# Optimization experiments

Measured on AMD Instinct MI355X. Metric: run time of the kernel, lower is better.

The kernel has to match this reference:

```python
import jax, jax.numpy as jnp
import numpy as np

B, C, H, W = 4, 128, 128, 128
E, K, HID = 11, 6, 512  # num_experts, active_experts, 4*dim


def setup_inputs() -> dict:
    key = jax.random.key(0)
    ks = jax.random.split(key, 5)
    return {
        "x": jax.random.normal(ks[0], (B, C, H, W), jnp.float32),
        "gate_w": jax.random.normal(ks[1], (E, C), jnp.float32) * 0.02,
        "gate_b": jnp.zeros((E,), jnp.float32),
        "w1": jax.random.normal(ks[2], (E, HID, C), jnp.float32) * 0.02,
        "b1": jnp.zeros((E, HID), jnp.float32),
        "w2": jax.random.normal(ks[3], (E, C, HID), jnp.float32) * 0.02,
        "b2": jnp.zeros((E, C), jnp.float32),
    }


def reference(x, gate_w, gate_b, w1, b1, w2, b2):
    n_experts = gate_w.shape[0]
    k = K  # active_experts
    # channels-last for per-pixel routing / 1x1-conv-as-matmul
    xcl = jnp.transpose(x, (0, 2, 3, 1))  # [B,H,W,C]
    # --- router (1x1 conv gate + softmax over experts + top-k) ---
    logits = jnp.einsum('bhwc,ec->bhwe', xcl, gate_w) + gate_b
    scores = jax.nn.softmax(logits, axis=-1)            # [B,H,W,E]
    topk_p, topk_i = jax.lax.top_k(scores, k)           # [B,H,W,K]
    topk_p = topk_p / topk_p.sum(axis=-1, keepdims=True)
    # scatter routing weights into dense per-expert mask (indices distinct)
    onehot = jax.nn.one_hot(topk_i, n_experts, dtype=x.dtype)  # [B,H,W,K,E]
    mask = jnp.einsum('bhwke,bhwk->bhwe', onehot, topk_p)      # [B,H,W,E]
    # --- dense expert compute, masked accumulate (as in original loop) ---
    acc = jnp.zeros_like(xcl)
    for e in range(n_experts):
        h = jax.nn.gelu(jnp.einsum('bhwc,dc->bhwd', xcl, w1[e]) + b1[e],
                        approximate=False)  # torch GELU is exact erf form
        oe = jnp.einsum('bhwd,cd->bhwc', h, w2[e]) + b2[e]
        acc = acc + mask[..., e:e + 1] * oe
    y = x + jnp.transpose(acc, (0, 3, 1, 2))  # back to NCHW
    # --- load-balancing aux loss ---
    mean_prob = scores.mean(axis=(0, 1, 2))            # [E]
    mean_load = onehot.sum(axis=3).mean(axis=(0, 1, 2))  # binary mask mean, [E]
    aux_loss = n_experts * jnp.sum(mean_prob * mean_load)
    return (y, aux_loss)
```

## Files before the change

### kernel.cpp

```cpp
#include <hip/hip_runtime.h>
#include <stdint.h>

#define C_   128
#define HW_  16384
#define CHW_ (C_*HW_)
#define N_   65536
#define E_   11
#define K_   6
#define HID_ 512

typedef __attribute__((ext_vector_type(8))) _Float16 half8;
typedef __attribute__((ext_vector_type(2))) _Float16 h2;
typedef __attribute__((ext_vector_type(2))) __fp16 fp16v2;
typedef __attribute__((ext_vector_type(16))) float float16v;
typedef __attribute__((ext_vector_type(2))) unsigned uint2v;

#define GLD(g, s) __builtin_amdgcn_global_load_lds( \
    (const __attribute__((address_space(1))) unsigned int*)(uintptr_t)(g), \
    (__attribute__((address_space(3))) unsigned int*)(unsigned int)(uintptr_t)(s), 16, 0, 0)

__device__ __forceinline__ h2 pkrtz(float a, float b){
  union { fp16v2 f; h2 h; } u;
  u.f = __builtin_amdgcn_cvt_pkrtz(a, b);
  return u.h;
}
__device__ __forceinline__ h2 gelu2h(h2 v, h2 wr2){
  h2 u = v * v;
  h2 s = u * (h2)(_Float16)(-0.00076957f) + (h2)(_Float16)(0.0147811f);
  s = s * u + (h2)(_Float16)(-0.126434f);
  s = s * u + (h2)(_Float16)(0.795742f);
  h2 p = v * s;
  h2 phi = p * (h2)(_Float16)(0.5f) + (h2)(_Float16)(0.5f);
  return v * wr2 * phi;
}
__device__ __forceinline__ void pswap32(unsigned &a, unsigned &b){
#if __has_builtin(__builtin_amdgcn_permlane32_swap)
  uint2v r = __builtin_amdgcn_permlane32_swap(a, b, false, false);
  a = r.x; b = r.y;
#else
  asm volatile("v_permlane32_swap_b32 %0, %1" : "+v"(a), "+v"(b));
#endif
}

__global__ __launch_bounds__(256) void k_convert(const float* __restrict__ w1,
                                                 const float* __restrict__ w2,
                                                 const float* __restrict__ b1,
                                                 unsigned short* __restrict__ wimg,
                                                 unsigned short* __restrict__ b1h,
                                                 float* __restrict__ auxsum){
  int t = blockIdx.x * 256 + threadIdx.x;
  if (t < 23) auxsum[t] = 0.0f;
  if (t >= 185856) return;
  if (t >= 180224){
    int t2 = t - 180224;
    int rec = t2 >> 5, j5 = t2 & 31;
    int hi = j5 >> 4, j = j5 & 15;
    int e = rec >> 4, hc = rec & 15;
    int row = (j & 3) + 8 * (j >> 2) + 4 * hi;
    union { _Float16 h; unsigned short u; } cv;
    cv.h = (_Float16)b1[e * 512 + hc * 32 + row];
    b1h[rec * 32 + j5] = cv.u;
    return;
  }
  const float* src;
  size_t dst;
  if (t < 90112){
    int e = t >> 13, hid = (t >> 4) & 511, c8 = t & 15;
    src = w1 + (size_t)t * 8;
    int rec = e * 16 + (hid >> 5);
    int kc = c8 >> 1, half = c8 & 1;
    int l = (hid & 31) | (half << 5);
    dst = (size_t)rec * 8192 + kc * 512 + l * 8;
  } else {
    int u = t - 90112;
    int e = u >> 13, cc = (u >> 6) & 127, hd8 = u & 63;
    src = w2 + (size_t)u * 8;
    int rec = e * 16 + (hd8 >> 2);
    int kc2 = (hd8 >> 1) & 1, half = hd8 & 1, ct = cc >> 5;
    int l = (cc & 31) | (half << 5);
    dst = (size_t)rec * 8192 + 4096 + (ct * 2 + kc2) * 512 + l * 8;
  }
  float4 a = *(const float4*)src, b = *(const float4*)(src + 4);
  union { _Float16 h[8]; uint4 v; } u4;
  u4.h[0] = (_Float16)a.x; u4.h[1] = (_Float16)a.y;
  u4.h[2] = (_Float16)a.z; u4.h[3] = (_Float16)a.w;
  u4.h[4] = (_Float16)b.x; u4.h[5] = (_Float16)b.y;
  u4.h[6] = (_Float16)b.z; u4.h[7] = (_Float16)b.w;
  *(uint4*)(wimg + dst) = u4.v;
}

__global__ __launch_bounds__(256) void k_pre(const float* __restrict__ x,
                                             const float* __restrict__ gw,
                                             const float* __restrict__ gb,
                                             const float* __restrict__ b2,
                                             unsigned short* __restrict__ xcl,
                                             float* __restrict__ mask,
                                             float* __restrict__ auxsum){
  __shared__ __align__(16) float tt[64 * 130];
  __shared__ __align__(16) float g[E_ * C_];
  __shared__ float gbs[E_];
  __shared__ float ap[E_], al[E_];
  int tid = threadIdx.x;
  int pix0 = blockIdx.x * 64;
  int b = pix0 >> 14, hw0 = pix0 & 16383;
  const float* xb = x + (size_t)b * CHW_ + hw0;

  for (int i = tid; i < E_ * C_; i += 256) g[i] = gw[i];
  if (tid < E_) { gbs[tid] = gb[tid]; ap[tid] = 0.f; al[tid] = 0.f; }

  #pragma unroll
  for (int it = 0; it < 8; ++it){
    int flat = it * 256 + tid;
    int c = flat >> 4, p4 = (flat & 15) << 2;
    float4 v = *(const float4*)(xb + (size_t)c * HW_ + p4);
    tt[(p4 + 0) * 130 + c] = v.x;
    tt[(p4 + 1) * 130 + c] = v.y;
    tt[(p4 + 2) * 130 + c] = v.z;
    tt[(p4 + 3) * 130 + c] = v.w;
  }
  __syncthreads();
  #pragma unroll 4
  for (int it = 0; it < 16; ++it){
    int u = it * 256 + tid;
    int p = u >> 6, cc = u & 63;
    float f0 = tt[p * 130 + 2 * cc], f1 = tt[p * 130 + 2 * cc + 1];
    union { h2 h; unsigned u; } pv;
    pv.h = pkrtz(f0, f1);
    ((unsigned*)xcl)[(size_t)(pix0 + p) * 64 + cc] = pv.u;
  }

  int p = tid >> 2, t4 = tid & 3;
  float lg[E_];
  #pragma unroll
  for (int e = 0; e < E_; ++e) lg[e] = (t4 == 0) ? gbs[e] : 0.f;
  const float2* ttrow = (const float2*)(tt + p * 130 + t4 * 32);
  #pragma unroll 4
  for (int j2 = 0; j2 < 16; ++j2){
    float2 xv = ttrow[j2];
    #pragma unroll
    for (int e = 0; e < E_; ++e){
      float2 gv = *(const float2*)(g + e * C_ + t4 * 32 + j2 * 2);
      lg[e] = fmaf(xv.x, gv.x, lg[e]);
      lg[e] = fmaf(xv.y, gv.y, lg[e]);
    }
  }
  #pragma unroll
  for (int e = 0; e < E_; ++e){
    lg[e] += __shfl_xor(lg[e], 1, 64);
    lg[e] += __shfl_xor(lg[e], 2, 64);
  }
  float mx = lg[0];
  #pragma unroll
  for (int e = 1; e < E_; ++e) mx = fmaxf(mx, lg[e]);
  float pr[E_]; float s = 0.f;
  #pragma unroll
  for (int e = 0; e < E_; ++e){ pr[e] = expf(lg[e] - mx); s += pr[e]; }
  float inv = 1.0f / s;
  #pragma unroll
  for (int e = 0; e < E_; ++e) pr[e] *= inv;

  unsigned selmask = 0; float wsum = 0.f;
  for (int k = 0; k < K_; ++k){
    float bv = -1.f; int bi = 0;
    #pragma unroll
    for (int e = 0; e < E_; ++e){
      bool better = (((selmask >> e) & 1u) == 0u) && (pr[e] > bv);
      bv = better ? pr[e] : bv;
      bi = better ? e : bi;
    }
    selmask |= 1u << bi; wsum += bv;
  }
  float invw = 1.0f / wsum;
  if (t4 == 0){
    int pix = pix0 + p;
    #pragma unroll
    for (int e = 0; e < E_; ++e){
      bool sel = (selmask >> e) & 1u;
      mask[(size_t)pix * E_ + e] = sel ? pr[e] * invw : 0.f;
      atomicAdd(&ap[e], pr[e]);
      if (sel) atomicAdd(&al[e], 1.0f);
    }
  }
  __syncthreads();
  if (tid < E_){
    atomicAdd(&auxsum[tid], ap[tid]);
    atomicAdd(&auxsum[E_ + tid], al[tid]);
  }
  if (blockIdx.x == 0 && tid < 64){
    int nz = 0;
    for (int idx = tid; idx < E_ * C_; idx += 64)
      nz |= (__float_as_uint(b2[idx]) != 0u) ? 1 : 0;
    if (nz) atomicOr((int*)(auxsum + 22), 1);
  }
}

__global__ __launch_bounds__(256, 2) void k_ffn(const unsigned short* __restrict__ xcl,
                                                const unsigned short* __restrict__ wimg,
                                                const unsigned short* __restrict__ b1h,
                                                const float* __restrict__ b2,
                                                const float* __restrict__ mask,
                                                const float* __restrict__ aux,
                                                const float* __restrict__ x,
                                                float* __restrict__ y){
  __shared__ unsigned char smem[65536];
  int tid = threadIdx.x;
  int w = tid >> 6, l = tid & 63;
  int l31 = l & 31, hi = l >> 5;
  int hi4 = hi * 4;
  int pix0 = blockIdx.x * 128;
  int off = (blockIdx.x % 11) * 16;
  const unsigned char* wimgB = (const unsigned char*)wimg;
  const unsigned char* b1hB  = (const unsigned char*)b1h;

  if (blockIdx.x == 0 && tid == 0){
    float s = 0.f;
    const float invN = 1.0f / (float)N_;
    for (int e = 0; e < E_; ++e)
      s += (aux[e] * invN) * (aux[E_ + e] * invN);
    y[(size_t)N_ * C_] = (float)E_ * s;
  }

  half8 Xf[8];
  {
    const unsigned short* xrow = xcl + ((size_t)(pix0 + w * 32 + l31) << 7) + hi * 8;
    #pragma unroll
    for (int kc = 0; kc < 8; ++kc)
      Xf[kc] = *(const half8*)(xrow + kc * 16);
  }

  uint4 bhA[4], bhB[4];
  const size_t mrow = (size_t)(pix0 + w * 32 + l31) * 11;

  {
    #pragma unroll
    for (int k = 0; k < 2; ++k){
      int rec = off + k;
      const unsigned char* gs = wimgB + (size_t)rec * 16384 + w * 4096 + l * 16;
      unsigned char* dst = smem + k * 16384 + w * 4096;
      GLD(gs, dst);               GLD(gs + 1024, dst + 1024);
      GLD(gs + 2048, dst + 2048); GLD(gs + 3072, dst + 3072);
    }
    #pragma unroll
    for (int k = 0; k < 2; ++k){
      int rec = off + k;
      const unsigned char* bp = b1hB + rec * 64 + hi * 32;
      bhA[2 * k]     = *(const uint4*)(bp);
      bhA[2 * k + 1] = *(const uint4*)(bp + 16);
    }
  }
  float wrn = mask[mrow + (off >> 4)];
  __syncthreads();

  float16v facc[4];
  #pragma unroll
  for (int ct = 0; ct < 4; ++ct) facc[ct] = (float16v)0.0f;
  h2 wr2 = (h2)(_Float16)0.0f;

#define REC_BODY(WB, BH0, BH1)                                                      \
  {                                                                                 \
    half8 a_[8];                                                                    \
    _Pragma("unroll")                                                               \
    for (int kc_ = 0; kc_ < 8; ++kc_)                                               \
      a_[kc_] = *(const half8*)((WB) + kc_ * 1024 + l * 16);                        \
    float16v hacc_ = (float16v)0.0f;                                                \
    __builtin_amdgcn_s_setprio(1);                                                  \
    _Pragma("unroll")                                                               \
    for (int kc_ = 0; kc_ < 8; ++kc_)                                               \
      hacc_ = __builtin_amdgcn_mfma_f32_32x32x16_f16(a_[kc_], Xf[kc_], hacc_, 0, 0, 0); \
    __builtin_amdgcn_s_setprio(0);                                                  \
    union { uint4 v[2]; h2 h[8]; } bu_;                                             \
    bu_.v[0] = BH0; bu_.v[1] = BH1;                                                 \
    unsigned pd_[8];                                                                \
    _Pragma("unroll")                                                               \
    for (int k_ = 0; k_ < 8; ++k_){                                                 \
      h2 v_ = pkrtz(hacc_[2 * k_], hacc_[2 * k_ + 1]);                              \
      v_ = v_ + bu_.h[k_];                                                          \
      union { h2 h; unsigned u; } g_;                                               \
      g_.h = gelu2h(v_, wr2);                                                       \
      pd_[k_] = g_.u;                                                               \
    }                                                                               \
    pswap32(pd_[0], pd_[2]); pswap32(pd_[1], pd_[3]);                               \
    pswap32(pd_[4], pd_[6]); pswap32(pd_[5], pd_[7]);                               \
    union { unsigned u[4]; half8 s; } cv0_, cv1_;                                   \
    cv0_.u[0] = pd_[0]; cv0_.u[1] = pd_[1]; cv0_.u[2] = pd_[2]; cv0_.u[3] = pd_[3]; \
    cv1_.u[0] = pd_[4]; cv1_.u[1] = pd_[5]; cv1_.u[2] = pd_[6]; cv1_.u[3] = pd_[7]; \
    half8 wv_[8];                                                                   \
    _Pragma("unroll")                                                               \
    for (int q_ = 0; q_ < 8; ++q_)                                                  \
      wv_[q_] = *(const half8*)((WB) + 8192 + q_ * 1024 + l * 16);                  \
    __builtin_amdgcn_s_setprio(1);                                                  \
    _Pragma("unroll")                                                               \
    for (int ct_ = 0; ct_ < 4; ++ct_){                                              \
      facc[ct_] = __builtin_amdgcn_mfma_f32_32x32x16_f16(wv_[2 * ct_],     cv0_.s, facc[ct_], 0, 0, 0); \
      facc[ct_] = __builtin_amdgcn_mfma_f32_32x32x16_f16(wv_[2 * ct_ + 1], cv1_.s, facc[ct_], 0, 0, 0); \
    }                                                                               \
    __builtin_amdgcn_s_setprio(0);                                                  \
  }

#define SUPER_BODY(J, BHC, BHL)                                                     \
  {                                                                                 \
    asm volatile("s_waitcnt vmcnt(4)" ::: "memory");                                \
    __builtin_amdgcn_s_barrier();                                                   \
    __builtin_amdgcn_sched_barrier(0);                                              \
         \
    {                                                                               \
      unsigned char* dbuf_ = smem + ((((J) + 1) & 1) << 15);                        \
      _Pragma("unroll")                                                             \
      for (int k_ = 0; k_ < 2; ++k_){                                               \
        int rn_ = 2 * (J) + 2 + k_ + off; if (rn_ >= 176) rn_ -= 176;               \
        const unsigned char* gs_ = wimgB + (size_t)rn_ * 16384 + w * 4096 + l * 16; \
        unsigned char* dst_ = dbuf_ + k_ * 16384 + w * 4096;                        \
        GLD(gs_, dst_);               GLD(gs_ + 1024, dst_ + 1024);                 \
        GLD(gs_ + 2048, dst_ + 2048); GLD(gs_ + 3072, dst_ + 3072);                 \
      }                                                                             \
      __builtin_amdgcn_sched_barrier(0);                                            \
      _Pragma("unroll")                                                             \
      for (int k_ = 0; k_ < 2; ++k_){                                               \
        int rn_ = 2 * (J) + 2 + k_ + off; if (rn_ >= 176) rn_ -= 176;               \
        const unsigned char* bp_ = b1hB + rn_ * 64 + hi * 32;                       \
        BHL[2 * k_]     = *(const uint4*)(bp_);                                     \
        BHL[2 * k_ + 1] = *(const uint4*)(bp_ + 16);                                \
      }                                                                             \
    }                                                                               \
    __builtin_amdgcn_sched_barrier(0);                                              \
    if (((J) & 7) == 0){           \
      _Float16 wh_ = (_Float16)wrn;                                                 \
      wr2 = (h2){wh_, wh_};                                                         \
      int rn_ = 2 * (J) + 16 + off; if (rn_ >= 176) rn_ -= 176;                     \
      wrn = mask[mrow + (rn_ >> 4)];                                                \
    }                                                                               \
    const unsigned char* wb_ = smem + (((J) & 1) << 15);                            \
    REC_BODY(wb_, BHC[0], BHC[1]);                                                  \
    REC_BODY(wb_ + 16384, BHC[2], BHC[3]);                                          \
  }

  #pragma unroll 1
  for (int jj = 0; jj < 44; ++jj){
    SUPER_BODY(2 * jj,     bhA, bhB);
    SUPER_BODY(2 * jj + 1, bhB, bhA);
  }
#undef SUPER_BODY
#undef REC_BODY

  __syncthreads();
  float* lds_t = (float*)smem;
  float* b2t   = (float*)(smem + 17408);
  for (int idx = tid; idx < 1536; idx += 256){
    int cc = idx / 12, ee = idx - cc * 12;
    b2t[idx] = (ee < 11) ? b2[ee * 128 + cc] : 0.f;
  }
  int b2nz = ((const int*)aux)[22];

  #pragma unroll 1
  for (int r = 0; r < 4; ++r){
    __syncthreads();
    if (w == r){
      #pragma unroll
      for (int ct = 0; ct < 4; ++ct)
        #pragma unroll
        for (int rg = 0; rg < 16; ++rg)
          lds_t[(ct * 32 + (rg & 3) + 8 * (rg >> 2) + hi4) * 33 + l31] = facc[ct][rg];
    }
    __syncthreads();
    int c = tid >> 1, ph = (tid & 1) << 4;
    int pixg = pix0 + r * 32 + ph;
    size_t base = (size_t)(pixg >> 14) * CHW_ + (size_t)c * HW_ + (pixg & 16383);
    float av[16];
    #pragma unroll
    for (int k = 0; k < 16; ++k) av[k] = lds_t[c * 33 + ph + k];
    if (b2nz){
      #pragma unroll
      for (int k = 0; k < 16; ++k){
        const float* mr = mask + (size_t)(pixg + k) * 11;
        #pragma unroll
        for (int e = 0; e < 11; ++e) av[k] = fmaf(mr[e], b2t[c * 12 + e], av[k]);
      }
    }
    #pragma unroll
    for (int q = 0; q < 4; ++q){
      float4 xv = *(const float4*)(x + base + q * 4);
      float4 o = {av[4 * q] + xv.x, av[4 * q + 1] + xv.y,
                  av[4 * q + 2] + xv.z, av[4 * q + 3] + xv.w};
      *(float4*)(y + base + q * 4) = o;
    }
  }
}

extern "C" void kernel_launch(void* const* d_in, const int* in_sizes, int n_in,
                              void* d_out, int out_size, void* d_ws, size_t ws_size,
                              hipStream_t stream){
  const float* x  = (const float*)d_in[0];
  const float* gw = (const float*)d_in[1];
  const float* gb = (const float*)d_in[2];
  const float* w1 = (const float*)d_in[3];
  const float* b1 = (const float*)d_in[4];
  const float* w2 = (const float*)d_in[5];
  const float* b2 = (const float*)d_in[6];
  float* y = (float*)d_out;
  char* ws = (char*)d_ws;

  unsigned short* xcl  = (unsigned short*)ws;
  unsigned short* wimg = (unsigned short*)(ws + 16777216);
  float* mask   = (float*)(ws + 19660800);
  float* auxsum = (float*)(ws + 22544384);
  unsigned short* b1h  = (unsigned short*)(ws + 22544480);

  hipLaunchKernelGGL(k_convert, dim3(726),  dim3(256), 0, stream, w1, w2, b1, wimg, b1h, auxsum);
  hipLaunchKernelGGL(k_pre,     dim3(1024), dim3(256), 0, stream, x, gw, gb, b2, xcl, mask, auxsum);
  hipLaunchKernelGGL(k_ffn,     dim3(512),  dim3(256), 0, stream, xcl, wimg, b1h, b2, mask, auxsum, x, y);
}
```

Before: 355.0 us.

## Software-pipeline two records so GELU epilogue overlaps MFMA chains

```diff
diff --git a/kernel.cpp b/kernel.cpp
--- a/kernel.cpp
+++ b/kernel.cpp
@@ -256,24 +256,14 @@
   for (int ct = 0; ct < 4; ++ct) facc[ct] = (float16v)0.0f;
   h2 wr2 = (h2)(_Float16)0.0f;
 
-#define REC_BODY(WB, BH0, BH1)                                                      \
+#define EPIC(HACC, BH0, BH1, CV0, CV1)                                              \
   {                                                                                 \
-    half8 a_[8];                                                                    \
-    _Pragma("unroll")                                                               \
-    for (int kc_ = 0; kc_ < 8; ++kc_)                                               \
-      a_[kc_] = *(const half8*)((WB) + kc_ * 1024 + l * 16);                        \
-    float16v hacc_ = (float16v)0.0f;                                                \
-    __builtin_amdgcn_s_setprio(1);                                                  \
-    _Pragma("unroll")                                                               \
-    for (int kc_ = 0; kc_ < 8; ++kc_)                                               \
-      hacc_ = __builtin_amdgcn_mfma_f32_32x32x16_f16(a_[kc_], Xf[kc_], hacc_, 0, 0, 0); \
-    __builtin_amdgcn_s_setprio(0);                                                  \
     union { uint4 v[2]; h2 h[8]; } bu_;                                             \
     bu_.v[0] = BH0; bu_.v[1] = BH1;                                                 \
     unsigned pd_[8];                                                                \
     _Pragma("unroll")                                                               \
     for (int k_ = 0; k_ < 8; ++k_){                                                 \
-      h2 v_ = pkrtz(hacc_[2 * k_], hacc_[2 * k_ + 1]);                              \
+      h2 v_ = pkrtz(HACC[2 * k_], HACC[2 * k_ + 1]);                                \
       v_ = v_ + bu_.h[k_];                                                          \
       union { h2 h; unsigned u; } g_;                                               \
       g_.h = gelu2h(v_, wr2);                                                       \
@@ -281,20 +271,10 @@
     }                                                                               \
     pswap32(pd_[0], pd_[2]); pswap32(pd_[1], pd_[3]);                               \
     pswap32(pd_[4], pd_[6]); pswap32(pd_[5], pd_[7]);                               \
-    union { unsigned u[4]; half8 s; } cv0_, cv1_;                                   \
-    cv0_.u[0] = pd_[0]; cv0_.u[1] = pd_[1]; cv0_.u[2] = pd_[2]; cv0_.u[3] = pd_[3]; \
-    cv1_.u[0] = pd_[4]; cv1_.u[1] = pd_[5]; cv1_.u[2] = pd_[6]; cv1_.u[3] = pd_[7]; \
-    half8 wv_[8];                                                                   \
-    _Pragma("unroll")                                                               \
-    for (int q_ = 0; q_ < 8; ++q_)                                                  \
-      wv_[q_] = *(const half8*)((WB) + 8192 + q_ * 1024 + l * 16);                  \
-    __builtin_amdgcn_s_setprio(1);                                                  \
-    _Pragma("unroll")                                                               \
-    for (int ct_ = 0; ct_ < 4; ++ct_){                                              \
-      facc[ct_] = __builtin_amdgcn_mfma_f32_32x32x16_f16(wv_[2 * ct_],     cv0_.s, facc[ct_], 0, 0, 0); \
-      facc[ct_] = __builtin_amdgcn_mfma_f32_32x32x16_f16(wv_[2 * ct_ + 1], cv1_.s, facc[ct_], 0, 0, 0); \
-    }                                                                               \
-    __builtin_amdgcn_s_setprio(0);                                                  \
+    union { unsigned u[4]; half8 s; } c0_, c1_;                                     \
+    c0_.u[0] = pd_[0]; c0_.u[1] = pd_[1]; c0_.u[2] = pd_[2]; c0_.u[3] = pd_[3];     \
+    c1_.u[0] = pd_[4]; c1_.u[1] = pd_[5]; c1_.u[2] = pd_[6]; c1_.u[3] = pd_[7];     \
+    CV0 = c0_.s; CV1 = c1_.s;                                                       \
   }
 
 #define SUPER_BODY(J, BHC, BHL)                                                     \
@@ -330,8 +310,59 @@
       wrn = mask[mrow + (rn_ >> 4)];                                                \
     }                                                                               \
     const unsigned char* wb_ = smem + (((J) & 1) << 15);                            \
-    REC_BODY(wb_, BHC[0], BHC[1]);                                                  \
-    REC_BODY(wb_ + 16384, BHC[2], BHC[3]);                                          \
+        \
+    half8 aA_[8], aB_[8];                                                           \
+    _Pragma("unroll")                                                               \
+    for (int q_ = 0; q_ < 8; ++q_){                                                 \
+      aA_[q_] = *(const half8*)(wb_ + q_ * 1024 + l * 16);                          \
+      aB_[q_] = *(const half8*)(wb_ + 16384 + q_ * 1024 + l * 16);                  \
+    }                                                                               \
+    float16v hA_ = (float16v)0.0f, hB_ = (float16v)0.0f;                            \
+    _Pragma("unroll")                                                               \
+    for (int kc_ = 0; kc_ < 8; ++kc_)                                               \
+      hA_ = __builtin_amdgcn_mfma_f32_32x32x16_f16(aA_[kc_], Xf[kc_], hA_, 0, 0, 0);\
+    __builtin_amdgcn_sched_barrier(0);                                              \
+                             \
+    _Pragma("unroll")                                                               \
+    for (int kc_ = 0; kc_ < 8; ++kc_)                                               \
+      hB_ = __builtin_amdgcn_mfma_f32_32x32x16_f16(aB_[kc_], Xf[kc_], hB_, 0, 0, 0);\
+    half8 cvA0_, cvA1_;                                                             \
+    EPIC(hA_, BHC[0], BHC[1], cvA0_, cvA1_);                                        \
+    _Pragma("unroll")                                                               \
+    for (int i_ = 0; i_ < 8; ++i_){                                                 \
+      __builtin_amdgcn_sched_group_barrier(0x008, 1, 0);               \
+      __builtin_amdgcn_sched_group_barrier(0x002, 11, 0);              \
+    }                                                                               \
+    __builtin_amdgcn_sched_barrier(0);                                              \
+                       \
+    half8 wvA_[8];                                                                  \
+    _Pragma("unroll")                                                               \
+    for (int q_ = 0; q_ < 8; ++q_)                                                  \
+      wvA_[q_] = *(const half8*)(wb_ + 8192 + q_ * 1024 + l * 16);                  \
+    half8 cvB0_, cvB1_;                                                             \
+    EPIC(hB_, BHC[2], BHC[3], cvB0_, cvB1_);                                        \
+    _Pragma("unroll")                                                               \
+    for (int ct_ = 0; ct_ < 4; ++ct_){                                              \
+      facc[ct_] = __builtin_amdgcn_mfma_f32_32x32x16_f16(wvA_[2 * ct_],     cvA0_, facc[ct_], 0, 0, 0); \
+      facc[ct_] = __builtin_amdgcn_mfma_f32_32x32x16_f16(wvA_[2 * ct_ + 1], cvA1_, facc[ct_], 0, 0, 0); \
+    }                                                                               \
+    _Pragma("unroll")                                                               \
+    for (int i_ = 0; i_ < 8; ++i_){                                                 \
+      __builtin_amdgcn_sched_group_barrier(0x100, 1, 0);             \
+      __builtin_amdgcn_sched_group_barrier(0x008, 1, 0);             \
+      __builtin_amdgcn_sched_group_barrier(0x002, 11, 0);            \
+    }                                                                               \
+    __builtin_amdgcn_sched_barrier(0);                                              \
+                                          \
+    half8 wvB_[8];                                                                  \
+    _Pragma("unroll")                                                               \
+    for (int q_ = 0; q_ < 8; ++q_)                                                  \
+      wvB_[q_] = *(const half8*)(wb_ + 16384 + 8192 + q_ * 1024 + l * 16);          \
+    _Pragma("unroll")                                                               \
+    for (int ct_ = 0; ct_ < 4; ++ct_){                                              \
+      facc[ct_] = __builtin_amdgcn_mfma_f32_32x32x16_f16(wvB_[2 * ct_],     cvB0_, facc[ct_], 0, 0, 0); \
+      facc[ct_] = __builtin_amdgcn_mfma_f32_32x32x16_f16(wvB_[2 * ct_ + 1], cvB1_, facc[ct_], 0, 0, 0); \
+    }                                                                               \
   }
 
   #pragma unroll 1
@@ -340,7 +371,7 @@
     SUPER_BODY(2 * jj + 1, bhB, bhA);
   }
 #undef SUPER_BODY
-#undef REC_BODY
+#undef EPIC
 
   __syncthreads();
   float* lds_t = (float*)smem;
```

Result: faster. 347.9 us (-2.0%).
